# Kernel tuning notes

Hardware: AMD Instinct MI355X
Metric: run time of the kernel (lower is better)

## Reference

```python
import jax, jax.numpy as jnp
import numpy as np

# dims: N batch, L seq, H heads, d projection_dim, P position_dimension
N, Lq, Lk, H, d, P = 2, 1024, 1024, 8, 64, 1
D = H * d


def _kernel(x):
    # _log_exp_kernel: positive feature map log(1+exp(x)) (softplus)
    return jax.nn.softplus(x)


def setup_inputs() -> dict:
    key = jax.random.key(0)
    ks = jax.random.split(key, 8)
    sc = 1.0 / np.sqrt(D).astype(np.float32)
    return {
        "query": jax.random.normal(ks[0], (N, Lq, D), jnp.float32),
        "key_seq": jax.random.normal(ks[1], (N, Lk, D), jnp.float32),
        "Wq": jax.random.normal(ks[2], (D, D), jnp.float32) * sc,
        "Wk": jax.random.normal(ks[3], (D, D), jnp.float32) * sc,
        "Wv": jax.random.normal(ks[4], (D, D), jnp.float32) * sc,
        "position_coeffs": jax.random.uniform(ks[5], (H, d), jnp.float32, 0.5, 1.5),
        "position_weight": jax.random.normal(ks[6], (H, d, P), jnp.float32) * 1e-3,
        "position_bias": jax.random.normal(ks[7], (H, d), jnp.float32) * 1e-2,
    }


def reference(query, key_seq, Wq, Wk, Wv, position_coeffs, position_weight, position_bias):
    # torch Linear (no bias): y = x @ W.T
    q = _kernel(jnp.einsum('nld,ed->nle', query, Wq).reshape(N, Lq, H, d))
    k = _kernel(jnp.einsum('nld,ed->nle', key_seq, Wk).reshape(N, Lk, H, d))
    v = jnp.einsum('nld,ed->nle', key_seq, Wv).reshape(N, Lk, H, d)
    # (N, H, L, d)
    q = jnp.transpose(q, (0, 2, 1, 3))
    k = jnp.transpose(k, (0, 2, 1, 3))
    v = jnp.transpose(v, (0, 2, 1, 3))

    # default positions: arange, query_offset = 0
    qpos = jnp.broadcast_to(jnp.arange(Lq, dtype=jnp.float32).reshape(1, Lq, 1), (N, Lq, P))
    kpos = jnp.broadcast_to(jnp.arange(Lk, dtype=jnp.float32).reshape(1, Lk, 1), (N, Lk, P))
    pq = jnp.einsum('nlp,hkp->nhlk', qpos, position_weight) + position_bias[None, :, None, :]
    pk = jnp.einsum('nlp,hkp->nhlk', kpos, position_weight)

    coeff = position_coeffs[None, :, None, :]  # (1, H, 1, d)

    def part(f, values):
        # causal (mask_future) linear attention via inclusive cumsum over keys
        Qf = q * f(pq) * coeff           # (N, H, Lq, d)
        Kf = k * f(pk)                   # (N, H, Lk, d)
        S = jnp.cumsum(jnp.einsum('nhkd,nhke->nhkde', Kf, values), axis=2)
        return jnp.einsum('nhqd,nhqde->nhqe', Qf, S)

    num = part(jnp.cos, v) + part(jnp.sin, v)           # (N, H, Lq, d)
    unit = jnp.ones((N, H, Lk, 1), jnp.float32)
    den = part(jnp.cos, unit) + part(jnp.sin, unit)     # (N, H, Lq, 1)
    attn = num / den
    return jnp.transpose(attn, (0, 2, 1, 3)).reshape(N, Lq, D)
```

## Files before the change

### kernel.cpp

```cpp
#include <hip/hip_runtime.h>
#include <cmath>

#define NB    2
#define LSEQ  1024
#define NH    8
#define HD    64
#define DD    512
#define FDIM  128
#define EV    65
#define CHUNK 64
#define NC    16
#define NBH   16

typedef short short8 __attribute__((ext_vector_type(8)));
typedef float floatx4 __attribute__((ext_vector_type(4)));

__device__ __forceinline__ float softplusf(float x) {
  return fmaxf(x, 0.0f) + log1pf(expf(-fabsf(x)));
}

__device__ __forceinline__ unsigned short f2bf(float f) {
  unsigned u = __float_as_uint(f);
  u += 0x7fffu + ((u >> 16) & 1u);
  return (unsigned short)(u >> 16);
}

__device__ __forceinline__ short8 cvt8(float4 a, float4 b) {
  short8 r;
  r[0] = (short)f2bf(a.x); r[1] = (short)f2bf(a.y);
  r[2] = (short)f2bf(a.z); r[3] = (short)f2bf(a.w);
  r[4] = (short)f2bf(b.x); r[5] = (short)f2bf(b.y);
  r[6] = (short)f2bf(b.z); r[7] = (short)f2bf(b.w);
  return r;
}

__global__ __launch_bounds__(256) void k_proj(
    const float* __restrict__ Xq, const float* __restrict__ Xkv,
    const float* __restrict__ Wq, const float* __restrict__ Wk,
    const float* __restrict__ Wv, const float* __restrict__ pw,
    const float* __restrict__ pb, const float* __restrict__ pc,
    float* __restrict__ Qf, float* __restrict__ Kf, float* __restrict__ Vx)
{
  __shared__ short Al[64][32];
  __shared__ short Bl[64][32];
  const int b = blockIdx.x;
  int m0, e0, pmode;
  const float *X, *W;
  if (b < 256) {
    m0 = (b >> 3) << 6; e0 = (b & 7) << 6;
    X = Xq; W = Wq + (size_t)e0 * DD; pmode = 0;
  } else {
    const int bb = b - 256;
    m0 = (bb >> 4) << 6;
    const int nt = bb & 15;
    e0 = (nt & 7) << 6;
    X = Xkv;
    if (nt < 8) { W = Wk + (size_t)e0 * DD; pmode = 1; }
    else        { W = Wv + (size_t)e0 * DD; pmode = 2; }
  }
  const int tid  = threadIdx.x;
  const int r    = tid >> 2;
  const int ko   = (tid & 3) << 3;
  const int wave = tid >> 6, lane = tid & 63;
  const int quad = lane >> 4, lm = lane & 15;
  const float* Ag = X + (size_t)(m0 + r) * DD + ko;
  const float* Bg = W + (size_t)r * DD + ko;
  floatx4 acc[4] = {};
  for (int k0 = 0; k0 < DD; k0 += 32) {
    const float4 a0 = *(const float4*)(Ag + k0);
    const float4 a1 = *(const float4*)(Ag + k0 + 4);
    const float4 b0 = *(const float4*)(Bg + k0);
    const float4 b1 = *(const float4*)(Bg + k0 + 4);
    __syncthreads();
    *(short8*)&Al[r][ko] = cvt8(a0, a1);
    *(short8*)&Bl[r][ko] = cvt8(b0, b1);
    __syncthreads();
    const short8 af = *(const short8*)&Al[(wave << 4) + lm][quad << 3];
#pragma unroll
    for (int t = 0; t < 4; ++t) {
      const short8 bf = *(const short8*)&Bl[(t << 4) + lm][quad << 3];
      acc[t] = __builtin_amdgcn_mfma_f32_16x16x32_bf16(af, bf, acc[t], 0, 0, 0);
    }
  }
#pragma unroll
  for (int t = 0; t < 4; ++t) {
    const int e = e0 + (t << 4) + lm;
    const int h = e >> 6, jj = e & 63;
    if (pmode == 2) {
#pragma unroll
      for (int rg = 0; rg < 4; ++rg) {
        const int m = m0 + (wave << 4) + (quad << 2) + rg;
        const int n = m >> 10, l = m & 1023;
        Vx[((size_t)(n * NH + h) * LSEQ + l) * HD + jj] = acc[t][rg];
      }
    } else {
      const float pwv = pw[e];
      const float pbv = (pmode == 0) ? pb[e] : 0.0f;
      const float pcv = (pmode == 0) ? pc[e] : 1.0f;
      float* base = (pmode == 0) ? Qf : Kf;
#pragma unroll
      for (int rg = 0; rg < 4; ++rg) {
        const int m = m0 + (wave << 4) + (quad << 2) + rg;
        const int n = m >> 10, l = m & 1023;
        const float v = softplusf(acc[t][rg]) * pcv;
        const float ang = fmaf((float)l, pwv, pbv);
        const float sn = __sinf(ang), cs = __cosf(ang);
        float* dst = &base[((size_t)(n * NH + h) * LSEQ + l) * FDIM + jj];
        dst[0]  = v * cs;
        dst[64] = v * sn;
      }
    }
  }
}

__global__ __launch_bounds__(256) void k_chunk_sums(
    const float* __restrict__ Kf, const float* __restrict__ Vx,
    float* __restrict__ S)
{
  const int c  = blockIdx.x & (NC - 1);
  const int bh = blockIdx.x >> 4;
  const int t0 = c * CHUNK;
  const int tid = threadIdx.x;
  __shared__ float Ks[CHUNK][FDIM];
  __shared__ float Vs[CHUNK][HD];
  for (int i = tid; i < CHUNK * (FDIM / 4); i += 256) {
    const int r = i >> 5, c4 = (i & 31) << 2;
    *(float4*)&Ks[r][c4] = *(const float4*)&Kf[((size_t)bh * LSEQ + t0 + r) * FDIM + c4];
  }
  for (int i = tid; i < CHUNK * (HD / 4); i += 256) {
    const int r = i >> 4, c4 = (i & 15) << 2;
    *(float4*)&Vs[r][c4] = *(const float4*)&Vx[((size_t)bh * LSEQ + t0 + r) * HD + c4];
  }
  __syncthreads();
  float* Sb = &S[(size_t)blockIdx.x * FDIM * EV];
  for (int task = tid; task < 32 * 17; task += 256) {
    const int ft = task & 31;
    const int et = task >> 5;
    const int f0 = ft << 2;
    if (et == 16) {
      float s[4] = {};
      for (int t = 0; t < CHUNK; ++t) {
        const float4 k4 = *(const float4*)&Ks[t][f0];
        s[0] += k4.x; s[1] += k4.y; s[2] += k4.z; s[3] += k4.w;
      }
#pragma unroll
      for (int u = 0; u < 4; ++u) Sb[(f0 + u) * EV + 64] = s[u];
    } else {
      const int e0 = et << 2;
      float a[4][4] = {};
      for (int t = 0; t < CHUNK; ++t) {
        const float4 k4 = *(const float4*)&Ks[t][f0];
        const float4 v4 = *(const float4*)&Vs[t][e0];
        const float kv[4] = {k4.x, k4.y, k4.z, k4.w};
        const float vv[4] = {v4.x, v4.y, v4.z, v4.w};
#pragma unroll
        for (int i = 0; i < 4; ++i)
#pragma unroll
          for (int j = 0; j < 4; ++j)
            a[i][j] = fmaf(kv[i], vv[j], a[i][j]);
      }
#pragma unroll
      for (int i = 0; i < 4; ++i)
#pragma unroll
        for (int j = 0; j < 4; ++j)
          Sb[(f0 + i) * EV + e0 + j] = a[i][j];
    }
  }
}

__global__ __launch_bounds__(256) void k_scan(float* __restrict__ S)
{
  const int bh = blockIdx.x >> 4;
  const int fg = blockIdx.x & 15;
  float* Sb = S + (size_t)bh * NC * FDIM * EV + (size_t)fg * 8 * EV;
  const size_t cs = (size_t)FDIM * EV;
  for (int i = threadIdx.x; i < 8 * EV; i += 256) {
    float* p = Sb + i;
    float v[NC];
#pragma unroll
    for (int c = 0; c < NC; ++c) v[c] = p[c * cs];
    float s = 0.0f;
#pragma unroll
    for (int c = 0; c < NC; ++c) { const float t = v[c]; p[c * cs] = s; s += t; }
  }
}

__global__ __launch_bounds__(256) void k_chunk_out(
    const float* __restrict__ Qf, const float* __restrict__ Kf,
    const float* __restrict__ Vx, const float* __restrict__ S,
    float* __restrict__ Out)
{
  const int c  = blockIdx.x & (NC - 1);
  const int bh = blockIdx.x >> 4;
  const int n  = bh >> 3, h = bh & 7;
  const int t0 = c * CHUNK;
  const int tid  = threadIdx.x;
  const int wave = tid >> 6, lane = tid & 63;
  const int quad = lane >> 4, lm = lane & 15;

  __shared__ short QL[64][128];
  __shared__ short KL[64][128];
  __shared__ short ScL[64][72];
  __shared__ short PT[80][136];
  __shared__ short VT[80][72];
  __shared__ float DenL[64];

  const float* Qg = &Qf[((size_t)bh * LSEQ + t0) * FDIM];
  const float* Kg = &Kf[((size_t)bh * LSEQ + t0) * FDIM];
  {
    const int f8 = (tid & 15) << 3;
#pragma unroll
    for (int rr = 0; rr < 64; rr += 16) {
      const int r = rr + (tid >> 4);
      const float4 a0 = *(const float4*)&Qg[r * FDIM + f8];
      const float4 a1 = *(const float4*)&Qg[r * FDIM + f8 + 4];
      *(short8*)&QL[r][f8] = cvt8(a0, a1);
      const float4 b0 = *(const float4*)&Kg[r * FDIM + f8];
      const float4 b1 = *(const float4*)&Kg[r * FDIM + f8 + 4];
      *(short8*)&KL[r][f8] = cvt8(b0, b1);
    }
  }
  {
    const float* Pg = &S[(size_t)(bh * NC + c) * FDIM * EV];
    for (int i = tid; i < FDIM * EV; i += 256) {
      const int f = i / EV, e = i - f * EV;
      PT[e][f] = (short)f2bf(Pg[i]);
    }
  }
  {
    const float* Vg = &Vx[((size_t)bh * LSEQ + t0) * HD];
    for (int i = tid; i < CHUNK * (HD / 4); i += 256) {
      const int t = i >> 4, e4 = (i & 15) << 2;
      const float4 v4 = *(const float4*)&Vg[t * HD + e4];
      VT[e4 + 0][t] = (short)f2bf(v4.x);
      VT[e4 + 1][t] = (short)f2bf(v4.y);
      VT[e4 + 2][t] = (short)f2bf(v4.z);
      VT[e4 + 3][t] = (short)f2bf(v4.w);
    }
    if (tid < CHUNK) VT[64][tid] = (short)0x3F80;
  }
  __syncthreads();

  short8 aQ[4];
#pragma unroll
  for (int ks = 0; ks < 4; ++ks)
    aQ[ks] = *(const short8*)&QL[(wave << 4) + lm][(quad << 3) + (ks << 5)];

  floatx4 accS[4] = {};
#pragma unroll
  for (int nt = 0; nt < 4; ++nt)
#pragma unroll
    for (int ks = 0; ks < 4; ++ks) {
      const short8 b = *(const short8*)&KL[(nt << 4) + lm][(quad << 3) + (ks << 5)];
      accS[nt] = __builtin_amdgcn_mfma_f32_16x16x32_bf16(aQ[ks], b, accS[nt], 0, 0, 0);
    }
#pragma unroll
  for (int nt = 0; nt < 4; ++nt)
#pragma unroll
    for (int rg = 0; rg < 4; ++rg) {
      const int m = (wave << 4) + (quad << 2) + rg;
      const int t = (nt << 4) + lm;
      ScL[m][t] = (short)((t <= m) ? f2bf(accS[nt][rg]) : 0);
    }

  floatx4 accN[5] = {};
#pragma unroll
  for (int nt = 0; nt < 5; ++nt)
#pragma unroll
    for (int ks = 0; ks < 4; ++ks) {
      const short8 b = *(const short8*)&PT[(nt << 4) + lm][(quad << 3) + (ks << 5)];
      accN[nt] = __builtin_amdgcn_mfma_f32_16x16x32_bf16(aQ[ks], b, accN[nt], 0, 0, 0);
    }

  short8 aS[2];
#pragma unroll
  for (int ks = 0; ks < 2; ++ks)
    aS[ks] = *(const short8*)&ScL[(wave << 4) + lm][(quad << 3) + (ks << 5)];
  floatx4 accV[5] = {};
#pragma unroll
  for (int nt = 0; nt < 5; ++nt)
#pragma unroll
    for (int ks = 0; ks < 2; ++ks) {
      const short8 b = *(const short8*)&VT[(nt << 4) + lm][(quad << 3) + (ks << 5)];
      accV[nt] = __builtin_amdgcn_mfma_f32_16x16x32_bf16(aS[ks], b, accV[nt], 0, 0, 0);
    }

  if (lm == 0) {
#pragma unroll
    for (int rg = 0; rg < 4; ++rg)
      DenL[(wave << 4) + (quad << 2) + rg] = accN[4][rg] + accV[4][rg];
  }

#pragma unroll
  for (int rg = 0; rg < 4; ++rg) {
    const int m = (wave << 4) + (quad << 2) + rg;
    const float rden = 1.0f / DenL[m];
    const int l = t0 + m;
#pragma unroll
    for (int nt = 0; nt < 4; ++nt) {
      const float val = (accN[nt][rg] + accV[nt][rg]) * rden;
      Out[((size_t)(n * LSEQ + l)) * DD + h * HD + (nt << 4) + lm] = val;
    }
  }
}

extern "C" void kernel_launch(void* const* d_in, const int* in_sizes, int n_in,
                              void* d_out, int out_size, void* d_ws, size_t ws_size,
                              hipStream_t stream) {
  (void)in_sizes; (void)n_in; (void)out_size; (void)ws_size;
  const float* query  = (const float*)d_in[0];
  const float* keyseq = (const float*)d_in[1];
  const float* Wq     = (const float*)d_in[2];
  const float* Wk     = (const float*)d_in[3];
  const float* Wv     = (const float*)d_in[4];
  const float* pc     = (const float*)d_in[5];
  const float* pw     = (const float*)d_in[6];
  const float* pb     = (const float*)d_in[7];
  float* out = (float*)d_out;

  float* ws = (float*)d_ws;
  float* Qf = ws;
  float* Kf = Qf + (size_t)NBH * LSEQ * FDIM;
  float* Vx = Kf + (size_t)NBH * LSEQ * FDIM;
  float* S  = Vx + (size_t)NBH * LSEQ * HD;

  k_proj      <<<768,      256, 0, stream>>>(query, keyseq, Wq, Wk, Wv, pw, pb, pc, Qf, Kf, Vx);
  k_chunk_sums<<<NBH * NC, 256, 0, stream>>>(Kf, Vx, S);
  k_scan      <<<NBH * NC, 256, 0, stream>>>(S);
  k_chunk_out <<<NBH * NC, 256, 0, stream>>>(Qf, Kf, Vx, S, out);
}
```

Measured before the change: 121.9 us.

## Use bf16 MFMA for chunk K^T V sums and double k-step with register prefetch in projection

The chunk-sum kernel now stages K and V transposed into LDS as bf16 and computes the per-chunk K^T[V|1] outer-product sums with MFMA instructions instead of scalar FMAs. It also splits the feature dimension across two blocks, doubling the grid. The projection GEMM now loads a 64-wide k-slab per iteration into padded LDS, prefetching the next slab into registers to overlap global loads with MFMA work. The bf16 rounding of K and V in the chunk sums adds precision loss compared with the fp32 accumulation before.

```diff
diff --git a/kernel.cpp b/kernel.cpp
--- a/kernel.cpp
+++ b/kernel.cpp
@@ -41,8 +41,8 @@
     const float* __restrict__ pb, const float* __restrict__ pc,
     float* __restrict__ Qf, float* __restrict__ Kf, float* __restrict__ Vx)
 {
-  __shared__ short Al[64][32];
-  __shared__ short Bl[64][32];
+  __shared__ short Al[64][72];
+  __shared__ short Bl[64][72];
   const int b = blockIdx.x;
   int m0, e0, pmode;
   const float *X, *W;
@@ -60,26 +60,40 @@
   }
   const int tid  = threadIdx.x;
   const int r    = tid >> 2;
-  const int ko   = (tid & 3) << 3;
+  const int ko   = (tid & 3) << 4;
   const int wave = tid >> 6, lane = tid & 63;
   const int quad = lane >> 4, lm = lane & 15;
   const float* Ag = X + (size_t)(m0 + r) * DD + ko;
   const float* Bg = W + (size_t)r * DD + ko;
+  float4 a[4], bb4[4];
+#pragma unroll
+  for (int u = 0; u < 4; ++u) {
+    a[u]   = *(const float4*)(Ag + (u << 2));
+    bb4[u] = *(const float4*)(Bg + (u << 2));
+  }
   floatx4 acc[4] = {};
-  for (int k0 = 0; k0 < DD; k0 += 32) {
-    const float4 a0 = *(const float4*)(Ag + k0);
-    const float4 a1 = *(const float4*)(Ag + k0 + 4);
-    const float4 b0 = *(const float4*)(Bg + k0);
-    const float4 b1 = *(const float4*)(Bg + k0 + 4);
+  for (int k0 = 0; k0 < DD; k0 += 64) {
     __syncthreads();
-    *(short8*)&Al[r][ko] = cvt8(a0, a1);
-    *(short8*)&Bl[r][ko] = cvt8(b0, b1);
+    *(short8*)&Al[r][ko]     = cvt8(a[0], a[1]);
+    *(short8*)&Al[r][ko + 8] = cvt8(a[2], a[3]);
+    *(short8*)&Bl[r][ko]     = cvt8(bb4[0], bb4[1]);
+    *(short8*)&Bl[r][ko + 8] = cvt8(bb4[2], bb4[3]);
     __syncthreads();
-    const short8 af = *(const short8*)&Al[(wave << 4) + lm][quad << 3];
-#pragma unroll
-    for (int t = 0; t < 4; ++t) {
-      const short8 bf = *(const short8*)&Bl[(t << 4) + lm][quad << 3];
-      acc[t] = __builtin_amdgcn_mfma_f32_16x16x32_bf16(af, bf, acc[t], 0, 0, 0);
+    if (k0 + 64 < DD) {
+#pragma unroll
+      for (int u = 0; u < 4; ++u) {
+        a[u]   = *(const float4*)(Ag + k0 + 64 + (u << 2));
+        bb4[u] = *(const float4*)(Bg + k0 + 64 + (u << 2));
+      }
+    }
+#pragma unroll
+    for (int ks = 0; ks < 2; ++ks) {
+      const short8 af = *(const short8*)&Al[(wave << 4) + lm][(quad << 3) + (ks << 5)];
+#pragma unroll
+      for (int t = 0; t < 4; ++t) {
+        const short8 bf = *(const short8*)&Bl[(t << 4) + lm][(quad << 3) + (ks << 5)];
+        acc[t] = __builtin_amdgcn_mfma_f32_16x16x32_bf16(af, bf, acc[t], 0, 0, 0);
+      }
     }
   }
 #pragma unroll
@@ -117,53 +131,64 @@
     const float* __restrict__ Kf, const float* __restrict__ Vx,
     float* __restrict__ S)
 {
-  const int c  = blockIdx.x & (NC - 1);
-  const int bh = blockIdx.x >> 4;
-  const int t0 = c * CHUNK;
-  const int tid = threadIdx.x;
-  __shared__ float Ks[CHUNK][FDIM];
-  __shared__ float Vs[CHUNK][HD];
-  for (int i = tid; i < CHUNK * (FDIM / 4); i += 256) {
-    const int r = i >> 5, c4 = (i & 31) << 2;
-    *(float4*)&Ks[r][c4] = *(const float4*)&Kf[((size_t)bh * LSEQ + t0 + r) * FDIM + c4];
-  }
-  for (int i = tid; i < CHUNK * (HD / 4); i += 256) {
-    const int r = i >> 4, c4 = (i & 15) << 2;
-    *(float4*)&Vs[r][c4] = *(const float4*)&Vx[((size_t)bh * LSEQ + t0 + r) * HD + c4];
-  }
+  const int blk = blockIdx.x;
+  const int bh  = blk >> 5;
+  const int c   = (blk >> 1) & (NC - 1);
+  const int fh  = blk & 1;
+  const int f0  = fh << 6;
+  const int t0  = c * CHUNK;
+  const int tid  = threadIdx.x;
+  const int wave = tid >> 6, lane = tid & 63;
+  const int quad = lane >> 4, lm = lane & 15;
+
+  __shared__ short KT[64][72];
+  __shared__ short VT[80][72];
+
+  for (int i = tid; i < 64 * 16; i += 256) {
+    const int t = i & 63, f4 = (i >> 6) << 2;
+    const float4 k4 = *(const float4*)&Kf[((size_t)bh * LSEQ + t0 + t) * FDIM + f0 + f4];
+    KT[f4 + 0][t] = (short)f2bf(k4.x);
+    KT[f4 + 1][t] = (short)f2bf(k4.y);
+    KT[f4 + 2][t] = (short)f2bf(k4.z);
+    KT[f4 + 3][t] = (short)f2bf(k4.w);
+  }
+  for (int i = tid; i < 64 * 16; i += 256) {
+    const int t = i & 63, e4 = (i >> 6) << 2;
+    const float4 v4 = *(const float4*)&Vx[((size_t)bh * LSEQ + t0 + t) * HD + e4];
+    VT[e4 + 0][t] = (short)f2bf(v4.x);
+    VT[e4 + 1][t] = (short)f2bf(v4.y);
+    VT[e4 + 2][t] = (short)f2bf(v4.z);
+    VT[e4 + 3][t] = (short)f2bf(v4.w);
+  }
+  if (tid < CHUNK) VT[64][tid] = (short)0x3F80;
   __syncthreads();
-  float* Sb = &S[(size_t)blockIdx.x * FDIM * EV];
-  for (int task = tid; task < 32 * 17; task += 256) {
-    const int ft = task & 31;
-    const int et = task >> 5;
-    const int f0 = ft << 2;
-    if (et == 16) {
-      float s[4] = {};
-      for (int t = 0; t < CHUNK; ++t) {
-        const float4 k4 = *(const float4*)&Ks[t][f0];
-        s[0] += k4.x; s[1] += k4.y; s[2] += k4.z; s[3] += k4.w;
-      }
-#pragma unroll
-      for (int u = 0; u < 4; ++u) Sb[(f0 + u) * EV + 64] = s[u];
-    } else {
-      const int e0 = et << 2;
-      float a[4][4] = {};
-      for (int t = 0; t < CHUNK; ++t) {
-        const float4 k4 = *(const float4*)&Ks[t][f0];
-        const float4 v4 = *(const float4*)&Vs[t][e0];
-        const float kv[4] = {k4.x, k4.y, k4.z, k4.w};
-        const float vv[4] = {v4.x, v4.y, v4.z, v4.w};
-#pragma unroll
-        for (int i = 0; i < 4; ++i)
-#pragma unroll
-          for (int j = 0; j < 4; ++j)
-            a[i][j] = fmaf(kv[i], vv[j], a[i][j]);
-      }
-#pragma unroll
-      for (int i = 0; i < 4; ++i)
-#pragma unroll
-        for (int j = 0; j < 4; ++j)
-          Sb[(f0 + i) * EV + e0 + j] = a[i][j];
+
+  short8 aK[2];
+#pragma unroll
+  for (int ks = 0; ks < 2; ++ks)
+    aK[ks] = *(const short8*)&KT[(wave << 4) + lm][(quad << 3) + (ks << 5)];
+  floatx4 acc[5] = {};
+#pragma unroll
+  for (int nt = 0; nt < 5; ++nt)
+#pragma unroll
+    for (int ks = 0; ks < 2; ++ks) {
+      const short8 bf = *(const short8*)&VT[(nt << 4) + lm][(quad << 3) + (ks << 5)];
+      acc[nt] = __builtin_amdgcn_mfma_f32_16x16x32_bf16(aK[ks], bf, acc[nt], 0, 0, 0);
+    }
+
+  float* Sb = &S[(size_t)(bh * NC + c) * FDIM * EV];
+#pragma unroll
+  for (int nt = 0; nt < 4; ++nt)
+#pragma unroll
+    for (int rg = 0; rg < 4; ++rg) {
+      const int f = f0 + (wave << 4) + (quad << 2) + rg;
+      Sb[f * EV + (nt << 4) + lm] = acc[nt][rg];
+    }
+  if (lm == 0) {
+#pragma unroll
+    for (int rg = 0; rg < 4; ++rg) {
+      const int f = f0 + (wave << 4) + (quad << 2) + rg;
+      Sb[f * EV + 64] = acc[4][rg];
     }
   }
 }
@@ -324,8 +349,8 @@
   float* Vx = Kf + (size_t)NBH * LSEQ * FDIM;
   float* S  = Vx + (size_t)NBH * LSEQ * HD;
 
-  k_proj      <<<768,      256, 0, stream>>>(query, keyseq, Wq, Wk, Wv, pw, pb, pc, Qf, Kf, Vx);
-  k_chunk_sums<<<NBH * NC, 256, 0, stream>>>(Kf, Vx, S);
-  k_scan      <<<NBH * NC, 256, 0, stream>>>(S);
-  k_chunk_out <<<NBH * NC, 256, 0, stream>>>(Qf, Kf, Vx, S, out);
-}
+  k_proj      <<<768,          256, 0, stream>>>(query, keyseq, Wq, Wk, Wv, pw, pb, pc, Qf, Kf, Vx);
+  k_chunk_sums<<<NBH * NC * 2, 256, 0, stream>>>(Kf, Vx, S);
+  k_scan      <<<NBH * NC,     256, 0, stream>>>(S);
+  k_chunk_out <<<NBH * NC,     256, 0, stream>>>(Qf, Kf, Vx, S, out);
+}
```

Result: faster. 119.4 us (-2.1%).
